# Optimization experiments

Hardware: AMD Instinct MI355X
Metric: run time of the kernel (lower is better)

Reference implementation:

```python
import jax, jax.numpy as jnp
import numpy as np

H = 1024       # hidden_dim
D_IN = 2048    # inner_dim
N = 16         # d_state
K = 4          # d_conv
R = 128        # dt_rank
EPS = 1e-6


def setup_inputs() -> dict:
    key = jax.random.key(0)
    ks = jax.random.split(key, 12)
    B, L = 2, 2048
    s = lambda *sh: 1.0 / np.sqrt(sh[-1])
    inp = {
        "x": jax.random.normal(ks[0], (B, L, H), jnp.float32),
        "norm_w": jnp.ones((H,), jnp.float32),
        "in_proj_w": jax.random.normal(ks[1], (2 * D_IN, H), jnp.float32) * s(H),
        "conv_w": jax.random.normal(ks[2], (D_IN, 1, K), jnp.float32) * s(K),
        "conv_b": jnp.zeros((D_IN,), jnp.float32),
        "x_proj_w": jax.random.normal(ks[3], (R + 2 * N, D_IN), jnp.float32) * s(D_IN),
        "dt_proj_w": jax.random.normal(ks[4], (D_IN, R), jnp.float32) * (D_IN ** -0.5),
        "dt_proj_b": jax.random.uniform(ks[5], (D_IN,), jnp.float32, 0.001, 0.1),
        "A_log": jnp.log(jnp.broadcast_to(jnp.arange(1, N + 1, dtype=jnp.float32), (D_IN, N))),
        "D_param": jnp.ones((D_IN,), jnp.float32),
        "out_proj_w": jax.random.normal(ks[6], (H, D_IN), jnp.float32) * s(D_IN),
    }
    return inp


def _rmsnorm(x, w):
    var = jnp.mean(jnp.square(x), axis=-1, keepdims=True)
    return x * jax.lax.rsqrt(var + EPS) * w


def _selective_scan(x, dt, Bm, Cm, A_log, D_param):
    # x, dt: (B, L, d); Bm, Cm: (B, L, N)
    A = -jnp.exp(A_log)  # (d, N)

    def step(h, inp):
        dt_t, B_t, C_t, x_t = inp  # (B,d),(B,N),(B,N),(B,d)
        dA = jnp.exp(dt_t[..., None] * A[None])           # (B,d,N)
        h = dA * h + (dt_t * x_t)[..., None] * B_t[:, None, :]
        y = jnp.einsum("bdn,bn->bd", h, C_t)
        return h, y

    B_, L_, d = x.shape
    h0 = jnp.zeros((B_, d, A.shape[1]), jnp.float32)
    xs = (dt.swapaxes(0, 1), Bm.swapaxes(0, 1), Cm.swapaxes(0, 1), x.swapaxes(0, 1))
    _, ys = jax.lax.scan(step, h0, xs)  # ys: (L, B, d)
    return ys.swapaxes(0, 1) + D_param * x


def reference(x, norm_w, in_proj_w, conv_w, conv_b, x_proj_w,
              dt_proj_w, dt_proj_b, A_log, D_param, out_proj_w):
    residual = x
    xn = _rmsnorm(x, norm_w)
    xz = xn @ in_proj_w.T                       # (B,L,2*D_IN)
    x_path, z_path = jnp.split(xz, 2, axis=-1)
    # causal depthwise conv1d
    xc = x_path.swapaxes(1, 2)                  # (B, D_IN, L)
    xc = jax.lax.conv_general_dilated(
        xc, conv_w, window_strides=(1,), padding=[(K - 1, 0)],
        feature_group_count=D_IN,
        dimension_numbers=("NCH", "OIH", "NCH"))
    xc = xc + conv_b[None, :, None]
    x_path = jax.nn.silu(xc.swapaxes(1, 2))     # (B, L, D_IN)
    x_dbl = x_path @ x_proj_w.T                 # (B, L, R+2N)
    dt_x, Bm, Cm = x_dbl[..., :R], x_dbl[..., R:R + N], x_dbl[..., R + N:]
    dt = jax.nn.softplus(dt_x @ dt_proj_w.T + dt_proj_b)
    y = _selective_scan(x_path.astype(jnp.float32), dt.astype(jnp.float32),
                        Bm.astype(jnp.float32), Cm.astype(jnp.float32),
                        A_log.astype(jnp.float32), D_param.astype(jnp.float32))
    y = y.astype(x.dtype) * jax.nn.silu(z_path)
    return y @ out_proj_w.T + residual
```

## Files before the change

kernel.cpp:

```cpp
#include <hip/hip_runtime.h>
#include <hip/hip_bf16.h>
#include <math.h>

typedef __bf16 bf16;
typedef bf16 bf16x8 __attribute__((ext_vector_type(8)));
typedef float f32x4 __attribute__((ext_vector_type(4)));

#define BLROWS 4096
#define HD 1024
#define DIN 2048
#define NST 16
#define RNK 128
#define LSEQ 2048
#define NC 64
#define LC 32
#define LOG2E 1.44269504088896f

__device__ __forceinline__ void gload_lds16(const void* g, void* l) {
  __builtin_amdgcn_global_load_lds(
      (const __attribute__((address_space(1))) unsigned int*)g,
      (__attribute__((address_space(3))) unsigned int*)l, 16, 0, 0);
}

__device__ __forceinline__ float silu_f(float x) {
  return x / (1.f + __expf(-x));
}

__device__ __forceinline__ float exp2_raw(float x) {
  return __builtin_amdgcn_exp2f(x);
}

__global__ __launch_bounds__(256) void cvt_all_kernel(const float* __restrict__ w0, bf16* __restrict__ o0,
                                                      const float* __restrict__ w1, bf16* __restrict__ o1,
                                                      const float* __restrict__ w2, bf16* __restrict__ o2,
                                                      const float* __restrict__ w3, bf16* __restrict__ o3) {
  int i = blockIdx.x * 256 + threadIdx.x;
  const float* s; bf16* d; int j;
  if (i < 1048576)      { s = w0; d = o0; j = i; }
  else if (i < 1130496) { s = w1; d = o1; j = i - 1048576; }
  else if (i < 1196032) { s = w2; d = o2; j = i - 1130496; }
  else                  { s = w3; d = o3; j = i - 1196032; }
  f32x4 v = *(const f32x4*)(s + (size_t)j * 4);
  bf16* o = d + (size_t)j * 4;
  o[0] = (bf16)v.x; o[1] = (bf16)v.y; o[2] = (bf16)v.z; o[3] = (bf16)v.w;
}

__global__ __launch_bounds__(256) void rmsnorm_kernel(const float* __restrict__ x,
                                                      const float* __restrict__ w,
                                                      bf16* __restrict__ xn) {
  int row = blockIdx.x;
  int t = threadIdx.x;
  const float* xr = x + (size_t)row * HD;
  f32x4 v = *(const f32x4*)(xr + t * 4);
  float s = v.x * v.x + v.y * v.y + v.z * v.z + v.w * v.w;
#pragma unroll
  for (int m = 1; m < 64; m <<= 1) s += __shfl_xor(s, m, 64);
  __shared__ float red[4];
  if ((t & 63) == 0) red[t >> 6] = s;
  __syncthreads();
  float tot = red[0] + red[1] + red[2] + red[3];
  float sc = rsqrtf(tot * (1.f / HD) + 1e-6f);
  const float* wr = w + t * 4;
  bf16* o = xn + (size_t)row * HD + t * 4;
  o[0] = (bf16)(v.x * sc * wr[0]);
  o[1] = (bf16)(v.y * sc * wr[1]);
  o[2] = (bf16)(v.z * sc * wr[2]);
  o[3] = (bf16)(v.w * sc * wr[3]);
}

enum { EPI_NONE = 0, EPI_SOFTPLUS = 1 };

template <int EPI, typename CT>
__global__ __launch_bounds__(256, 2) void gemm_bt(const bf16* __restrict__ A,
                                                  const bf16* __restrict__ B,
                                                  CT* __restrict__ C,
                                                  const float* __restrict__ bias,
                                                  int M, int N, int ldab, int Kslice,
                                                  int ldc, long long strideC) {
  __shared__ __align__(16) bf16 lA[128 * 64];
  __shared__ __align__(16) bf16 lB[128 * 64];
  const int tid = threadIdx.x;
  const int wave = tid >> 6;
  const int lane = tid & 63;
  const int m0 = blockIdx.y * 128;
  const int n0 = blockIdx.x * 128;
  const int kz = blockIdx.z;
  const bf16* Ab = A + (size_t)kz * Kslice;
  const bf16* Bb = B + (size_t)kz * Kslice;
  CT* Cb = C + (size_t)kz * strideC;
  const int wr = wave >> 1, wc = wave & 1;
  f32x4 acc[4][4] = {};
  const int lrow = lane >> 3;
  const int lcole = (lane & 7) * 8;

  for (int k0 = 0; k0 < Kslice; k0 += 64) {
#pragma unroll
    for (int j = 0; j < 4; ++j) {
      int chunk = wave * 4 + j;
      int row = chunk * 8 + lrow;
      gload_lds16(Ab + (size_t)(m0 + row) * ldab + k0 + lcole, lA + chunk * 512);
      gload_lds16(Bb + (size_t)(n0 + row) * ldab + k0 + lcole, lB + chunk * 512);
    }
    __syncthreads();
#pragma unroll
    for (int kk = 0; kk < 64; kk += 32) {
      bf16x8 af[4], bfr[4];
      const int kof = kk + ((lane >> 4) * 8);
#pragma unroll
      for (int i = 0; i < 4; ++i)
        af[i] = *(const bf16x8*)&lA[(wr * 64 + i * 16 + (lane & 15)) * 64 + kof];
#pragma unroll
      for (int j = 0; j < 4; ++j)
        bfr[j] = *(const bf16x8*)&lB[(wc * 64 + j * 16 + (lane & 15)) * 64 + kof];
#pragma unroll
      for (int i = 0; i < 4; ++i)
#pragma unroll
        for (int j = 0; j < 4; ++j)
          acc[i][j] = __builtin_amdgcn_mfma_f32_16x16x32_bf16(af[i], bfr[j], acc[i][j], 0, 0, 0);
    }
    __syncthreads();
  }

  const int crow0 = (lane >> 4) * 4;
  const int ccol = lane & 15;
#pragma unroll
  for (int i = 0; i < 4; ++i) {
#pragma unroll
    for (int j = 0; j < 4; ++j) {
      int col = n0 + wc * 64 + j * 16 + ccol;
      if (col >= N) continue;
#pragma unroll
      for (int v = 0; v < 4; ++v) {
        int row = m0 + wr * 64 + i * 16 + crow0 + v;
        float val = acc[i][j][v];
        if (EPI == EPI_SOFTPLUS) {
          val += bias[col];
          val = (val > 20.f) ? val : log1pf(expf(val));
        }
        Cb[(size_t)row * ldc + col] = (CT)val;
      }
    }
  }
}

__global__ __launch_bounds__(256, 2) void gemm_resid64(const bf16* __restrict__ A,
                                                       const bf16* __restrict__ B,
                                                       float* __restrict__ C,
                                                       const float* __restrict__ resid,
                                                       int K, int ldc) {
  __shared__ __align__(16) bf16 lA[128 * 64];
  __shared__ __align__(16) bf16 lB[64 * 64];
  const int tid = threadIdx.x;
  const int wave = tid >> 6;
  const int lane = tid & 63;
  const int m0 = blockIdx.y * 128;
  const int n0 = blockIdx.x * 64;
  const int wr = wave >> 1, wc = wave & 1;
  f32x4 acc[4][2] = {};
  const int lrow = lane >> 3;
  const int lcole = (lane & 7) * 8;

  for (int k0 = 0; k0 < K; k0 += 64) {
#pragma unroll
    for (int j = 0; j < 4; ++j) {
      int chunk = wave * 4 + j;
      int row = chunk * 8 + lrow;
      gload_lds16(A + (size_t)(m0 + row) * K + k0 + lcole, lA + chunk * 512);
    }
#pragma unroll
    for (int j = 0; j < 2; ++j) {
      int chunk = wave * 2 + j;
      int row = chunk * 8 + lrow;
      gload_lds16(B + (size_t)(n0 + row) * K + k0 + lcole, lB + chunk * 512);
    }
    __syncthreads();
#pragma unroll
    for (int kk = 0; kk < 64; kk += 32) {
      bf16x8 af[4], bfr[2];
      const int kof = kk + ((lane >> 4) * 8);
#pragma unroll
      for (int i = 0; i < 4; ++i)
        af[i] = *(const bf16x8*)&lA[(wr * 64 + i * 16 + (lane & 15)) * 64 + kof];
#pragma unroll
      for (int j = 0; j < 2; ++j)
        bfr[j] = *(const bf16x8*)&lB[(wc * 32 + j * 16 + (lane & 15)) * 64 + kof];
#pragma unroll
      for (int i = 0; i < 4; ++i)
#pragma unroll
        for (int j = 0; j < 2; ++j)
          acc[i][j] = __builtin_amdgcn_mfma_f32_16x16x32_bf16(af[i], bfr[j], acc[i][j], 0, 0, 0);
    }
    __syncthreads();
  }

  const int crow0 = (lane >> 4) * 4;
  const int ccol = lane & 15;
#pragma unroll
  for (int i = 0; i < 4; ++i) {
#pragma unroll
    for (int j = 0; j < 2; ++j) {
      int col = n0 + wc * 32 + j * 16 + ccol;
#pragma unroll
      for (int v = 0; v < 4; ++v) {
        int row = m0 + wr * 64 + i * 16 + crow0 + v;
        C[(size_t)row * ldc + col] = acc[i][j][v] + resid[(size_t)row * ldc + col];
      }
    }
  }
}

__global__ __launch_bounds__(256) void conv_silu_kernel(const bf16* __restrict__ xz,
                                                        const float* __restrict__ cw,
                                                        const float* __restrict__ cb,
                                                        bf16* __restrict__ xcb) {
  int i8 = blockIdx.x * 256 + threadIdx.x;
  int d8 = i8 & 255;
  int bl = i8 >> 8;
  int l = bl & (LSEQ - 1);
  const bf16* base = xz + (size_t)bl * 4096 + d8 * 8;
  float acc[8];
  {
    const f32x4* cbp = (const f32x4*)(cb + d8 * 8);
    f32x4 c0 = cbp[0], c1 = cbp[1];
    acc[0] = c0.x; acc[1] = c0.y; acc[2] = c0.z; acc[3] = c0.w;
    acc[4] = c1.x; acc[5] = c1.y; acc[6] = c1.z; acc[7] = c1.w;
  }
  const f32x4* cwp = (const f32x4*)(cw + (size_t)d8 * 32);
#pragma unroll
  for (int k = 0; k < 4; ++k) {
    int ll = l - 3 + k;
    if (ll < 0) continue;
    bf16x8 v = *(const bf16x8*)(base + (ptrdiff_t)(k - 3) * 4096);
#pragma unroll
    for (int dd = 0; dd < 8; ++dd) acc[dd] += (float)v[dd] * cwp[dd][k];
  }
  bf16x8 o;
#pragma unroll
  for (int dd = 0; dd < 8; ++dd) o[dd] = (bf16)silu_f(acc[dd]);
  *(bf16x8*)(xcb + (size_t)bl * DIN + d8 * 8) = o;
}

__global__ __launch_bounds__(256) void reduce_xdbl_kernel(const float* __restrict__ part,
                                                          bf16* __restrict__ dtx,
                                                          float* __restrict__ bcb) {
  int r = blockIdx.x;
  int t = threadIdx.x;
  if (t >= 160) return;
  size_t o = (size_t)r * 160 + t;
  float s = part[o] + part[o + 655360] + part[o + 2 * 655360] + part[o + 3 * 655360];
  if (t < 128) dtx[(size_t)r * 128 + t] = (bf16)s;
  else bcb[(size_t)r * 32 + (t - 128)] = s;
}


__global__ __launch_bounds__(256) void scan_p1(const bf16* __restrict__ dt,
                                               const bf16* __restrict__ xc,
                                               const float* __restrict__ bcb,
                                               const float* __restrict__ A_log,
                                               float* __restrict__ sumP,
                                               float* __restrict__ sumQ) {
  const int idx = blockIdx.x;
  const int dtile = idx & 15;
  const int c = (idx >> 4) & (NC - 1);
  const int b = idx >> 10;
  const int t = threadIdx.x;
  const int d = dtile * 128 + (t >> 1);
  const int half = t & 1;
  const size_t rowbase = (size_t)(b * LSEQ + c * LC);

  __shared__ __align__(16) f32x4 s_b[LC * 4];
  if (t < LC * 4) {
    int l = t >> 2, q = t & 3;
    s_b[t] = ((const f32x4*)(bcb + (rowbase + l) * 32))[q];
  }
  __syncthreads();

  float Acoef2[8];
  {
    const f32x4* Ap = (const f32x4*)(A_log + (size_t)d * 16 + half * 8);
#pragma unroll
    for (int q = 0; q < 2; ++q) {
      f32x4 av = Ap[q];
      Acoef2[q * 4 + 0] = -LOG2E * __expf(av.x);
      Acoef2[q * 4 + 1] = -LOG2E * __expf(av.y);
      Acoef2[q * 4 + 2] = -LOG2E * __expf(av.z);
      Acoef2[q * 4 + 3] = -LOG2E * __expf(av.w);
    }
  }

  float h[8];
#pragma unroll
  for (int n = 0; n < 8; ++n) h[n] = 0.f;
  float dtsum = 0.f;

  const bf16* dtp = dt + rowbase * DIN + d;
  const bf16* xp  = xc + rowbase * DIN + d;
#pragma unroll 4
  for (int l = 0; l < LC; ++l) {
    float dtv = (float)dtp[(size_t)l * DIN];
    float xv  = (float)xp[(size_t)l * DIN];
    float du = dtv * xv;
    dtsum += dtv;
    float Bl[8];
    *(f32x4*)&Bl[0] = s_b[l * 4 + half * 2 + 0];
    *(f32x4*)&Bl[4] = s_b[l * 4 + half * 2 + 1];
#pragma unroll
    for (int n = 0; n < 8; ++n) {
      float dA = exp2_raw(dtv * Acoef2[n]);
      h[n] = dA * h[n] + du * Bl[n];
    }
  }

  f32x4* op = (f32x4*)(sumP + ((size_t)(b * NC + c) * DIN + d) * 16 + half * 8);
  f32x4* oq = (f32x4*)(sumQ + ((size_t)(b * NC + c) * DIN + d) * 16 + half * 8);
#pragma unroll
  for (int q = 0; q < 2; ++q) {
    f32x4 pv, qv;
    pv.x = exp2_raw(dtsum * Acoef2[q * 4 + 0]);
    pv.y = exp2_raw(dtsum * Acoef2[q * 4 + 1]);
    pv.z = exp2_raw(dtsum * Acoef2[q * 4 + 2]);
    pv.w = exp2_raw(dtsum * Acoef2[q * 4 + 3]);
    qv.x = h[q * 4 + 0]; qv.y = h[q * 4 + 1]; qv.z = h[q * 4 + 2]; qv.w = h[q * 4 + 3];
    op[q] = pv; oq[q] = qv;
  }
}

__global__ __launch_bounds__(256) void scan_p2(const float* __restrict__ sumP,
                                               float* __restrict__ sumQ) {
  int tid = blockIdx.x * 256 + threadIdx.x;
  int b = tid >> 15;
  int dn = tid & 32767;
  size_t o = (size_t)b * NC * DIN * 16 + dn;
  float h = 0.f;
  float Pv = sumP[o], Qv = sumQ[o];
  for (int c = 0; c < NC; ++c) {
    size_t on = o + DIN * 16;
    float Pn = 0.f, Qn = 0.f;
    if (c < NC - 1) { Pn = sumP[on]; Qn = sumQ[on]; }
    sumQ[o] = h;
    h = fmaf(Pv, h, Qv);
    Pv = Pn; Qv = Qn; o = on;
  }
}

__global__ __launch_bounds__(256) void scan_p3(const bf16* __restrict__ dt,
                                               const bf16* __restrict__ xc,
                                               const float* __restrict__ bcb,
                                               const float* __restrict__ A_log,
                                               const float* __restrict__ hin,
                                               const bf16* __restrict__ xz,
                                               const float* __restrict__ Dp,
                                               bf16* __restrict__ y) {
  const int idx = blockIdx.x;
  const int dtile = idx & 15;
  const int c = (idx >> 4) & (NC - 1);
  const int b = idx >> 10;
  const int t = threadIdx.x;
  const int d = dtile * 128 + (t >> 1);
  const int half = t & 1;
  const size_t rowbase = (size_t)(b * LSEQ + c * LC);

  __shared__ __align__(16) f32x4 s_bc[LC * 8];
  {
    int l = t >> 3, q = t & 7;
    s_bc[t] = ((const f32x4*)(bcb + (rowbase + l) * 32))[q];
  }
  __syncthreads();

  float Acoef2[8];
  {
    const f32x4* Ap = (const f32x4*)(A_log + (size_t)d * 16 + half * 8);
#pragma unroll
    for (int q = 0; q < 2; ++q) {
      f32x4 av = Ap[q];
      Acoef2[q * 4 + 0] = -LOG2E * __expf(av.x);
      Acoef2[q * 4 + 1] = -LOG2E * __expf(av.y);
      Acoef2[q * 4 + 2] = -LOG2E * __expf(av.z);
      Acoef2[q * 4 + 3] = -LOG2E * __expf(av.w);
    }
  }

  float h[8];
  {
    const f32x4* hp = (const f32x4*)(hin + ((size_t)(b * NC + c) * DIN + d) * 16 + half * 8);
#pragma unroll
    for (int q = 0; q < 2; ++q) {
      f32x4 hv = hp[q];
      h[q * 4 + 0] = hv.x; h[q * 4 + 1] = hv.y; h[q * 4 + 2] = hv.z; h[q * 4 + 3] = hv.w;
    }
  }
  float Dv = Dp[d];

  const bf16* dtp = dt + rowbase * DIN + d;
  const bf16* xp  = xc + rowbase * DIN + d;
  const bf16* zp  = xz + rowbase * 4096 + DIN + d;
  bf16* yp = y + rowbase * DIN + d;

#pragma unroll 4
  for (int l = 0; l < LC; ++l) {
    float dtv = (float)dtp[(size_t)l * DIN];
    float xv  = (float)xp[(size_t)l * DIN];
    float zv  = (float)zp[(size_t)l * 4096];
    float du = dtv * xv;
    float Bl[8], Cl[8];
    *(f32x4*)&Bl[0] = s_bc[l * 8 + half * 2 + 0];
    *(f32x4*)&Bl[4] = s_bc[l * 8 + half * 2 + 1];
    *(f32x4*)&Cl[0] = s_bc[l * 8 + 4 + half * 2 + 0];
    *(f32x4*)&Cl[4] = s_bc[l * 8 + 4 + half * 2 + 1];
    float yv = 0.f;
#pragma unroll
    for (int n = 0; n < 8; ++n) {
      float dA = exp2_raw(dtv * Acoef2[n]);
      h[n] = dA * h[n] + du * Bl[n];
      yv += h[n] * Cl[n];
    }
    yv += __shfl_xor(yv, 1, 64);
    if (half == 0) {
      float outv = (yv + Dv * xv) * silu_f(zv);
      yp[(size_t)l * DIN] = (bf16)outv;
    }
  }
}

extern "C" void kernel_launch(void* const* d_in, const int* in_sizes, int n_in,
                              void* d_out, int out_size, void* d_ws, size_t ws_size,
                              hipStream_t stream) {
  const float* x = (const float*)d_in[0];
  const float* norm_w = (const float*)d_in[1];
  const float* in_proj_w = (const float*)d_in[2];
  const float* conv_w = (const float*)d_in[3];
  const float* conv_b = (const float*)d_in[4];
  const float* x_proj_w = (const float*)d_in[5];
  const float* dt_proj_w = (const float*)d_in[6];
  const float* dt_proj_b = (const float*)d_in[7];
  const float* A_log = (const float*)d_in[8];
  const float* D_param = (const float*)d_in[9];
  const float* out_proj_w = (const float*)d_in[10];
  float* out = (float*)d_out;

  size_t off = 0;
  char* wsb = (char*)d_ws;
  auto alloc = [&](size_t bytes) {
    void* p = wsb + off;
    off += (bytes + 255) & ~(size_t)255;
    return p;
  };
  bf16* xn = (bf16*)alloc((size_t)BLROWS * HD * 2);
  bf16* w_in = (bf16*)alloc((size_t)4096 * HD * 2);
  bf16* xzb = (bf16*)alloc((size_t)BLROWS * 4096 * 2);
  bf16* xcb = (bf16*)alloc((size_t)BLROWS * DIN * 2);
  bf16* xpw = (bf16*)alloc((size_t)256 * DIN * 2);
  float* part2 = (float*)alloc((size_t)4 * BLROWS * 160 * 4);
  bf16* dtx = (bf16*)alloc((size_t)BLROWS * RNK * 2);
  float* bcb = (float*)alloc((size_t)BLROWS * 32 * 4);
  bf16* dtw = (bf16*)alloc((size_t)DIN * RNK * 2);
  bf16* dtf = (bf16*)alloc((size_t)BLROWS * DIN * 2);
  bf16* yb = (bf16*)alloc((size_t)BLROWS * DIN * 2);
  bf16* outw = (bf16*)alloc((size_t)HD * DIN * 2);
  float* sumP = (float*)alloc((size_t)2 * NC * DIN * NST * 4);
  float* sumQ = (float*)alloc((size_t)2 * NC * DIN * NST * 4);
  (void)ws_size; (void)n_in; (void)in_sizes; (void)out_size;

  cvt_all_kernel<<<6720, 256, 0, stream>>>(in_proj_w, w_in, x_proj_w, xpw,
                                           dt_proj_w, dtw, out_proj_w, outw);

  rmsnorm_kernel<<<BLROWS, 256, 0, stream>>>(x, norm_w, xn);

  gemm_bt<EPI_NONE, bf16><<<dim3(32, 32, 1), 256, 0, stream>>>(
      xn, w_in, xzb, nullptr, BLROWS, 4096, HD, HD, 4096, 0);

  conv_silu_kernel<<<4096, 256, 0, stream>>>(xzb, conv_w, conv_b, xcb);

  gemm_bt<EPI_NONE, float><<<dim3(2, 32, 4), 256, 0, stream>>>(
      xcb, xpw, part2, nullptr, BLROWS, 160, DIN, 512, 160, (long long)BLROWS * 160);

  reduce_xdbl_kernel<<<BLROWS, 256, 0, stream>>>(part2, dtx, bcb);

  gemm_bt<EPI_SOFTPLUS, bf16><<<dim3(16, 32, 1), 256, 0, stream>>>(
      dtx, dtw, dtf, dt_proj_b, BLROWS, DIN, RNK, RNK, DIN, 0);

  scan_p1<<<2 * NC * 16, 256, 0, stream>>>(dtf, xcb, bcb, A_log, sumP, sumQ);
  scan_p2<<<(2 * DIN * NST) / 256, 256, 0, stream>>>(sumP, sumQ);
  scan_p3<<<2 * NC * 16, 256, 0, stream>>>(dtf, xcb, bcb, A_log, sumQ, xzb, D_param, yb);

  gemm_resid64<<<dim3(16, 32), 256, 0, stream>>>(yb, outw, out, x, DIN, HD);
}
```

Baseline: 376.3 us.

## Add 256x256 triple-buffered in_proj GEMM, fuse prep kernels, shrink scan carry data

The in_proj GEMM moves to a new 512-thread kernel with 256x256 tiles, a three-stage direct-to-LDS pipeline, swizzled LDS layout, wave priority hints and XCD-aware block remapping. The rmsnorm and weight-conversion kernels are merged into one launch to save a launch and a tail. The chunked scan now stores only the per-chunk dt sum instead of 16 decay factors and recomputes the exp2 in pass 2, which cuts memory traffic. The new GEMM uses 96KB of dynamic shared memory, which limits occupancy, and writes its C tile with scattered scalar bf16 stores.

```diff
diff --git a/kernel.cpp b/kernel.cpp
--- a/kernel.cpp
+++ b/kernel.cpp
@@ -30,42 +30,150 @@
   return __builtin_amdgcn_exp2f(x);
 }
 
-__global__ __launch_bounds__(256) void cvt_all_kernel(const float* __restrict__ w0, bf16* __restrict__ o0,
-                                                      const float* __restrict__ w1, bf16* __restrict__ o1,
-                                                      const float* __restrict__ w2, bf16* __restrict__ o2,
-                                                      const float* __restrict__ w3, bf16* __restrict__ o3) {
-  int i = blockIdx.x * 256 + threadIdx.x;
-  const float* s; bf16* d; int j;
-  if (i < 1048576)      { s = w0; d = o0; j = i; }
-  else if (i < 1130496) { s = w1; d = o1; j = i - 1048576; }
-  else if (i < 1196032) { s = w2; d = o2; j = i - 1130496; }
-  else                  { s = w3; d = o3; j = i - 1196032; }
-  f32x4 v = *(const f32x4*)(s + (size_t)j * 4);
-  bf16* o = d + (size_t)j * 4;
-  o[0] = (bf16)v.x; o[1] = (bf16)v.y; o[2] = (bf16)v.z; o[3] = (bf16)v.w;
-}
-
-__global__ __launch_bounds__(256) void rmsnorm_kernel(const float* __restrict__ x,
-                                                      const float* __restrict__ w,
-                                                      bf16* __restrict__ xn) {
-  int row = blockIdx.x;
-  int t = threadIdx.x;
-  const float* xr = x + (size_t)row * HD;
-  f32x4 v = *(const f32x4*)(xr + t * 4);
-  float s = v.x * v.x + v.y * v.y + v.z * v.z + v.w * v.w;
-#pragma unroll
-  for (int m = 1; m < 64; m <<= 1) s += __shfl_xor(s, m, 64);
-  __shared__ float red[4];
-  if ((t & 63) == 0) red[t >> 6] = s;
-  __syncthreads();
-  float tot = red[0] + red[1] + red[2] + red[3];
-  float sc = rsqrtf(tot * (1.f / HD) + 1e-6f);
-  const float* wr = w + t * 4;
-  bf16* o = xn + (size_t)row * HD + t * 4;
-  o[0] = (bf16)(v.x * sc * wr[0]);
-  o[1] = (bf16)(v.y * sc * wr[1]);
-  o[2] = (bf16)(v.z * sc * wr[2]);
-  o[3] = (bf16)(v.w * sc * wr[3]);
+__device__ __forceinline__ int swz_off(int row, int colbyte) {
+  int w = ((row & 15) << 6) | colbyte;
+  w ^= ((w >> 9) & 1) << 5;
+  return ((row >> 4) << 10) | w;
+}
+
+__global__ __launch_bounds__(256) void prep_kernel(
+    const float* __restrict__ x, const float* __restrict__ nw, bf16* __restrict__ xn,
+    const float* __restrict__ w0, bf16* __restrict__ o0,
+    const float* __restrict__ w1, bf16* __restrict__ o1,
+    const float* __restrict__ w2, bf16* __restrict__ o2,
+    const float* __restrict__ w3, bf16* __restrict__ o3) {
+  const int t = threadIdx.x;
+  if (blockIdx.x < BLROWS) {
+    const int row = blockIdx.x;
+    const float* xr = x + (size_t)row * HD;
+    f32x4 v = *(const f32x4*)(xr + t * 4);
+    float s = v.x * v.x + v.y * v.y + v.z * v.z + v.w * v.w;
+#pragma unroll
+    for (int m = 1; m < 64; m <<= 1) s += __shfl_xor(s, m, 64);
+    __shared__ float red[4];
+    if ((t & 63) == 0) red[t >> 6] = s;
+    __syncthreads();
+    float tot = red[0] + red[1] + red[2] + red[3];
+    float sc = rsqrtf(tot * (1.f / HD) + 1e-6f);
+    const float* wr = nw + t * 4;
+    bf16* o = xn + (size_t)row * HD + t * 4;
+    o[0] = (bf16)(v.x * sc * wr[0]);
+    o[1] = (bf16)(v.y * sc * wr[1]);
+    o[2] = (bf16)(v.z * sc * wr[2]);
+    o[3] = (bf16)(v.w * sc * wr[3]);
+  } else {
+    int i = (blockIdx.x - BLROWS) * 256 + t;
+    const float* s; bf16* d; int j;
+    if (i < 1048576)      { s = w0; d = o0; j = i; }
+    else if (i < 1130496) { s = w1; d = o1; j = i - 1048576; }
+    else if (i < 1196032) { s = w2; d = o2; j = i - 1130496; }
+    else                  { s = w3; d = o3; j = i - 1196032; }
+    f32x4 v = *(const f32x4*)(s + (size_t)j * 4);
+    bf16* o = d + (size_t)j * 4;
+    o[0] = (bf16)v.x; o[1] = (bf16)v.y; o[2] = (bf16)v.z; o[3] = (bf16)v.w;
+  }
+}
+
+__global__ __launch_bounds__(512, 2) void gemm8_bt(const bf16* __restrict__ A,
+                                                   const bf16* __restrict__ B,
+                                                   bf16* __restrict__ C,
+                                                   int M, int N, int K) {
+  extern __shared__ char smem[];
+  const int tid = threadIdx.x;
+  int nwg = gridDim.x;
+  int wg = (blockIdx.x & 7) * (nwg >> 3) + (blockIdx.x >> 3);
+  const int mtiles = M >> 8;
+  const int m0 = (wg % mtiles) * 256;
+  const int n0 = (wg / mtiles) * 256;
+  const int wave = tid >> 6, lane = tid & 63;
+  const int wr = wave >> 2, wc = wave & 3;
+  const int frow = lane & 15;
+  const int kbyte = ((lane >> 4) << 3) * 2;
+  const int waveb = wave << 10;
+  const int nt = K >> 5;
+
+  auto stage = [&](int slot, int k0) {
+    char* base = smem + slot * 32768;
+#pragma unroll
+    for (int h = 0; h < 2; ++h) {
+      int o = tid * 16 + h * 8192;
+      int w = o & 1023;
+      int w2 = w ^ (((w >> 9) & 1) << 5);
+      int row = ((o >> 10) << 4) | (w2 >> 6);
+      int col = (w2 & 63) >> 1;
+      int ldso = waveb + h * 8192;
+      gload_lds16(A + (size_t)(m0 + row) * K + k0 + col, base + ldso);
+      gload_lds16(B + (size_t)(n0 + row) * K + k0 + col, base + 16384 + ldso);
+    }
+  };
+
+  stage(0, 0); stage(1, 32); stage(2, 64);
+  asm volatile("s_waitcnt vmcnt(8)" ::: "memory");
+  __builtin_amdgcn_s_barrier();
+  asm volatile("" ::: "memory");
+
+  f32x4 acc[8][4] = {};
+  int cur = 0;
+  for (int t = 0; t < nt; ++t) {
+    const char* sA = smem + cur * 32768;
+    const char* sB = sA + 16384;
+    bf16x8 bfr[4], af[4];
+#pragma unroll
+    for (int j = 0; j < 4; ++j)
+      bfr[j] = *(const bf16x8*)(sB + swz_off(wc * 64 + j * 16 + frow, kbyte));
+#pragma unroll
+    for (int i = 0; i < 4; ++i)
+      af[i] = *(const bf16x8*)(sA + swz_off(wr * 128 + i * 16 + frow, kbyte));
+    __builtin_amdgcn_s_setprio(1);
+#pragma unroll
+    for (int i = 0; i < 4; ++i)
+#pragma unroll
+      for (int j = 0; j < 4; ++j)
+        acc[i][j] = __builtin_amdgcn_mfma_f32_16x16x32_bf16(af[i], bfr[j], acc[i][j], 0, 0, 0);
+    __builtin_amdgcn_s_setprio(0);
+    asm volatile("" ::: "memory");
+    __builtin_amdgcn_s_barrier();
+    asm volatile("" ::: "memory");
+#pragma unroll
+    for (int i = 0; i < 4; ++i)
+      af[i] = *(const bf16x8*)(sA + swz_off(wr * 128 + (i + 4) * 16 + frow, kbyte));
+    __builtin_amdgcn_s_setprio(1);
+#pragma unroll
+    for (int i = 0; i < 4; ++i)
+#pragma unroll
+      for (int j = 0; j < 4; ++j)
+        acc[i + 4][j] = __builtin_amdgcn_mfma_f32_16x16x32_bf16(af[i], bfr[j], acc[i + 4][j], 0, 0, 0);
+    __builtin_amdgcn_s_setprio(0);
+    asm volatile("" ::: "memory");
+    __builtin_amdgcn_s_barrier();
+    asm volatile("" ::: "memory");
+    if (t + 3 < nt) {
+      stage(cur, (t + 3) << 5);
+      asm volatile("s_waitcnt vmcnt(8)" ::: "memory");
+    } else if (t == nt - 3) {
+      asm volatile("s_waitcnt vmcnt(4)" ::: "memory");
+    } else if (t == nt - 2) {
+      asm volatile("s_waitcnt vmcnt(0)" ::: "memory");
+    }
+    __builtin_amdgcn_s_barrier();
+    asm volatile("" ::: "memory");
+    cur = (cur == 2) ? 0 : cur + 1;
+  }
+
+  const int ccol = lane & 15;
+  const int crow0 = (lane >> 4) << 2;
+#pragma unroll
+  for (int i = 0; i < 8; ++i) {
+#pragma unroll
+    for (int j = 0; j < 4; ++j) {
+      int col = n0 + wc * 64 + j * 16 + ccol;
+#pragma unroll
+      for (int v = 0; v < 4; ++v) {
+        int row = m0 + wr * 128 + i * 16 + crow0 + v;
+        C[(size_t)row * N + col] = (bf16)acc[i][j][v];
+      }
+    }
+  }
 }
 
 enum { EPI_NONE = 0, EPI_SOFTPLUS = 1 };
@@ -252,12 +360,11 @@
   else bcb[(size_t)r * 32 + (t - 128)] = s;
 }
 
-
 __global__ __launch_bounds__(256) void scan_p1(const bf16* __restrict__ dt,
                                                const bf16* __restrict__ xc,
                                                const float* __restrict__ bcb,
                                                const float* __restrict__ A_log,
-                                               float* __restrict__ sumP,
+                                               float* __restrict__ dsum,
                                                float* __restrict__ sumQ) {
   const int idx = blockIdx.x;
   const int dtile = idx & 15;
@@ -311,35 +418,35 @@
     }
   }
 
-  f32x4* op = (f32x4*)(sumP + ((size_t)(b * NC + c) * DIN + d) * 16 + half * 8);
+  if (half == 0) dsum[(size_t)(b * NC + c) * DIN + d] = dtsum;
   f32x4* oq = (f32x4*)(sumQ + ((size_t)(b * NC + c) * DIN + d) * 16 + half * 8);
 #pragma unroll
   for (int q = 0; q < 2; ++q) {
-    f32x4 pv, qv;
-    pv.x = exp2_raw(dtsum * Acoef2[q * 4 + 0]);
-    pv.y = exp2_raw(dtsum * Acoef2[q * 4 + 1]);
-    pv.z = exp2_raw(dtsum * Acoef2[q * 4 + 2]);
-    pv.w = exp2_raw(dtsum * Acoef2[q * 4 + 3]);
+    f32x4 qv;
     qv.x = h[q * 4 + 0]; qv.y = h[q * 4 + 1]; qv.z = h[q * 4 + 2]; qv.w = h[q * 4 + 3];
-    op[q] = pv; oq[q] = qv;
-  }
-}
-
-__global__ __launch_bounds__(256) void scan_p2(const float* __restrict__ sumP,
+    oq[q] = qv;
+  }
+}
+
+__global__ __launch_bounds__(256) void scan_p2(const float* __restrict__ dsum,
+                                               const float* __restrict__ A_log,
                                                float* __restrict__ sumQ) {
   int tid = blockIdx.x * 256 + threadIdx.x;
   int b = tid >> 15;
   int dn = tid & 32767;
+  int d = dn >> 4;
+  float Ac = -LOG2E * __expf(A_log[dn]);
   size_t o = (size_t)b * NC * DIN * 16 + dn;
+  size_t os = (size_t)b * NC * DIN + d;
   float h = 0.f;
-  float Pv = sumP[o], Qv = sumQ[o];
+  float sv = dsum[os], Qv = sumQ[o];
   for (int c = 0; c < NC; ++c) {
     size_t on = o + DIN * 16;
-    float Pn = 0.f, Qn = 0.f;
-    if (c < NC - 1) { Pn = sumP[on]; Qn = sumQ[on]; }
+    float sn = 0.f, Qn = 0.f;
+    if (c < NC - 1) { sn = dsum[os + DIN]; Qn = sumQ[on]; }
     sumQ[o] = h;
-    h = fmaf(Pv, h, Qv);
-    Pv = Pn; Qv = Qn; o = on;
+    h = fmaf(exp2_raw(sv * Ac), h, Qv);
+    sv = sn; Qv = Qn; o = on; os += DIN;
   }
 }
 
@@ -457,17 +564,18 @@
   bf16* dtf = (bf16*)alloc((size_t)BLROWS * DIN * 2);
   bf16* yb = (bf16*)alloc((size_t)BLROWS * DIN * 2);
   bf16* outw = (bf16*)alloc((size_t)HD * DIN * 2);
-  float* sumP = (float*)alloc((size_t)2 * NC * DIN * NST * 4);
+  float* dsum = (float*)alloc((size_t)2 * NC * DIN * 4);
   float* sumQ = (float*)alloc((size_t)2 * NC * DIN * NST * 4);
   (void)ws_size; (void)n_in; (void)in_sizes; (void)out_size;
 
-  cvt_all_kernel<<<6720, 256, 0, stream>>>(in_proj_w, w_in, x_proj_w, xpw,
-                                           dt_proj_w, dtw, out_proj_w, outw);
-
-  rmsnorm_kernel<<<BLROWS, 256, 0, stream>>>(x, norm_w, xn);
-
-  gemm_bt<EPI_NONE, bf16><<<dim3(32, 32, 1), 256, 0, stream>>>(
-      xn, w_in, xzb, nullptr, BLROWS, 4096, HD, HD, 4096, 0);
+  hipFuncSetAttribute((const void*)gemm8_bt,
+                      hipFuncAttributeMaxDynamicSharedMemorySize, 98304);
+
+  prep_kernel<<<BLROWS + 6720, 256, 0, stream>>>(x, norm_w, xn,
+                                                 in_proj_w, w_in, x_proj_w, xpw,
+                                                 dt_proj_w, dtw, out_proj_w, outw);
+
+  gemm8_bt<<<256, 512, 98304, stream>>>(xn, w_in, xzb, BLROWS, 4096, HD);
 
   conv_silu_kernel<<<4096, 256, 0, stream>>>(xzb, conv_w, conv_b, xcb);
 
@@ -479,8 +587,8 @@
   gemm_bt<EPI_SOFTPLUS, bf16><<<dim3(16, 32, 1), 256, 0, stream>>>(
       dtx, dtw, dtf, dt_proj_b, BLROWS, DIN, RNK, RNK, DIN, 0);
 
-  scan_p1<<<2 * NC * 16, 256, 0, stream>>>(dtf, xcb, bcb, A_log, sumP, sumQ);
-  scan_p2<<<(2 * DIN * NST) / 256, 256, 0, stream>>>(sumP, sumQ);
+  scan_p1<<<2 * NC * 16, 256, 0, stream>>>(dtf, xcb, bcb, A_log, dsum, sumQ);
+  scan_p2<<<(2 * DIN * NST) / 256, 256, 0, stream>>>(dsum, A_log, sumQ);
   scan_p3<<<2 * NC * 16, 256, 0, stream>>>(dtf, xcb, bcb, A_log, sumQ, xzb, D_param, yb);
 
   gemm_resid64<<<dim3(16, 32), 256, 0, stream>>>(yb, outw, out, x, DIN, HD);
```

New measurement: 367.9 us. -2.3%, faster.
